# Kernel optimization log

Measured on AMD Instinct MI355X. Metric: run time of the kernel, lower is better.

## Reference

```python
import jax, jax.numpy as jnp
import numpy as np

N, D, K = 500000, 256, 64

def setup_inputs() -> dict:
    key = jax.random.key(0)
    kq, km = jax.random.split(key)
    query = jax.random.normal(kq, (D,), dtype=jnp.float32)
    mat = jax.random.normal(km, (N, D), dtype=jnp.float32)
    return {"query": query, "mat": mat, "k": K}

def reference(query, mat, k):
    # scores = mat @ query  : [N]
    scores = jnp.einsum("nd,d->n", mat, query)
    # top-k selection over all stored vectors
    _, idx = jax.lax.top_k(scores, k)
    # gather the selected rows : [k, D]
    out = jnp.take(mat, idx, axis=0)
    # idx stands in for the metadata gather (meta[i] for i in idx)
    return out, idx
```

## Files before the change

### kernel.cpp

```cpp
#include <hip/hip_runtime.h>
#include <stdint.h>

#define DIM 256
#define TOPK 64
#define HIST_BINS 65536
#define CAP 4096

__device__ __forceinline__ uint32_t fkey(float f) {
  uint32_t u = __float_as_uint(f);
  return (u & 0x80000000u) ? ~u : (u | 0x80000000u);
}

__global__ __launch_bounds__(256) void zero_kernel(uint32_t* __restrict__ hist,
                                                   int* __restrict__ cnt) {
  int tid = blockIdx.x * 256 + threadIdx.x;
  ((uint4*)hist)[tid] = make_uint4(0u, 0u, 0u, 0u);
  if (tid == 0) *cnt = 0;
}

__global__ __launch_bounds__(256) void score_kernel(
    const float* __restrict__ mat, const float* __restrict__ query,
    float* __restrict__ scores, uint32_t* __restrict__ hist, int n) {
  const int lane = threadIdx.x & 63;
  const int li = lane & 15;
  const int sub = lane >> 4;
  const int gw = blockIdx.x * 4 + (threadIdx.x >> 6);
  const int W = gridDim.x * 4;

  float4 q0 = ((const float4*)query)[li];
  float4 q1 = ((const float4*)query)[li + 16];
  float4 q2 = ((const float4*)query)[li + 32];
  float4 q3 = ((const float4*)query)[li + 48];

  int n4 = (n + 3) >> 2;
  for (int r4 = gw; r4 < n4; r4 += W) {
    int row = r4 * 4 + sub;
    float d = 0.f;
    if (row < n) {
      const float4* m4 = (const float4*)(mat + (size_t)row * DIM);
      float4 a = m4[li];
      float4 b = m4[li + 16];
      float4 c = m4[li + 32];
      float4 e = m4[li + 48];
      d = a.x * q0.x + a.y * q0.y + a.z * q0.z + a.w * q0.w;
      d += b.x * q1.x + b.y * q1.y + b.z * q1.z + b.w * q1.w;
      d += c.x * q2.x + c.y * q2.y + c.z * q2.z + c.w * q2.w;
      d += e.x * q3.x + e.y * q3.y + e.z * q3.z + e.w * q3.w;
    }
#pragma unroll
    for (int off = 8; off > 0; off >>= 1) d += __shfl_xor(d, off, 64);
    if (li == 0 && row < n) {
      scores[row] = d;
      atomicAdd(&hist[fkey(d) >> 16], 1u);
    }
  }
}

__global__ __launch_bounds__(256) void thresh_kernel(
    const uint32_t* __restrict__ hist, int* __restrict__ tbin) {
  __shared__ uint32_t s[256];
  __shared__ int fc;
  __shared__ uint32_t above;
  int t = threadIdx.x;

  uint32_t acc = 0;
  const uint4* h4 = (const uint4*)(hist + t * 256);
  for (int j = 0; j < 64; ++j) {
    uint4 v = h4[j];
    acc += v.x + v.y + v.z + v.w;
  }
  s[t] = acc;
  __syncthreads();
  for (int off = 1; off < 256; off <<= 1) {
    uint32_t v = (t + off < 256) ? s[t + off] : 0u;
    __syncthreads();
    s[t] += v;
    __syncthreads();
  }
  if (s[t] >= TOPK && (t == 255 || s[t + 1] < TOPK)) {
    fc = t;
    above = (t == 255) ? 0u : s[t + 1];
  }
  __syncthreads();
  int c = fc;
  uint32_t a = above;
  uint32_t h = hist[c * 256 + t];
  __syncthreads();
  s[t] = h;
  __syncthreads();
  for (int off = 1; off < 256; off <<= 1) {
    uint32_t v = (t + off < 256) ? s[t + off] : 0u;
    __syncthreads();
    s[t] += v;
    __syncthreads();
  }
  if (a + s[t] >= TOPK && (t == 255 || a + s[t + 1] < TOPK)) {
    *tbin = c * 256 + t;
  }
}

__global__ __launch_bounds__(256) void collect_kernel(
    const float* __restrict__ scores, const int* __restrict__ tbin,
    int* __restrict__ cnt, unsigned long long* __restrict__ cand, int n) {
  uint32_t T = (uint32_t)(*tbin);
  int i = blockIdx.x * 256 + threadIdx.x;
  int stride = gridDim.x * 256;
  for (; i < n; i += stride) {
    uint32_t key = fkey(scores[i]);
    if ((key >> 16) >= T) {
      int pos = atomicAdd(cnt, 1);
      if (pos < CAP) {
        cand[pos] = ((unsigned long long)key << 32) | (uint32_t)(~(uint32_t)i);
      }
    }
  }
}

__global__ __launch_bounds__(1024) void final_kernel(
    const unsigned long long* __restrict__ cand, const int* __restrict__ cnt,
    const float* __restrict__ mat, float* __restrict__ out) {
  __shared__ unsigned long long c[CAP];
  __shared__ int sel[TOPK];
  int t = threadIdx.x;
  int M = *cnt;
  if (M > CAP) M = CAP;

  for (int i = t; i < M; i += 1024) c[i] = cand[i];
  __syncthreads();

  for (int i = t; i < M; i += 1024) {
    unsigned long long mykey = c[i];
    int rank = 0;
    for (int j = 0; j < M; ++j) rank += (c[j] > mykey) ? 1 : 0;
    if (rank < TOPK) sel[rank] = (int)(~(uint32_t)(mykey & 0xFFFFFFFFull));
  }
  __syncthreads();

  if (t < TOPK) out[TOPK * DIM + t] = (float)sel[t];

  int wv = t >> 6, lane = t & 63;
  for (int r = wv; r < TOPK; r += 16) {
    size_t row = (size_t)sel[r];
    float4 v = ((const float4*)(mat + row * DIM))[lane];
    ((float4*)(out + r * DIM))[lane] = v;
  }
}

extern "C" void kernel_launch(void* const* d_in, const int* in_sizes, int n_in,
                              void* d_out, int out_size, void* d_ws, size_t ws_size,
                              hipStream_t stream) {
  const float* query = (const float*)d_in[0];
  const float* mat = (const float*)d_in[1];
  float* out = (float*)d_out;
  int n = in_sizes[1] / DIM;

  char* ws = (char*)d_ws;
  float* scores = (float*)ws;
  uint32_t* hist = (uint32_t*)(ws + (2u << 20));
  int* tbin = (int*)(ws + (2u << 20) + HIST_BINS * 4);
  int* cnt = tbin + 1;
  unsigned long long* cand =
      (unsigned long long*)(ws + (2u << 20) + HIST_BINS * 4 + 16);

  zero_kernel<<<64, 256, 0, stream>>>(hist, cnt);
  score_kernel<<<2048, 256, 0, stream>>>(mat, query, scores, hist, n);
  thresh_kernel<<<1, 256, 0, stream>>>(hist, tbin);
  collect_kernel<<<512, 256, 0, stream>>>(scores, tbin, cnt, cand, n);
  final_kernel<<<1, 1024, 0, stream>>>(cand, cnt, mat, out);
}
```

Before: 765.5 us.

## Process two rows per subgroup in scoring and fuse threshold into collect

The score kernel now has each 16-lane subgroup load and reduce two rows per iteration, putting more loads in flight. The grid size is computed from n rather than fixed. The single-block threshold kernel is removed and every collect block recomputes the threshold bin from the histogram, which saves one launch and its serialisation. The cost is that all 512 collect blocks each read the 256KB histogram redundantly.

```diff
diff --git a/kernel.cpp b/kernel.cpp
--- a/kernel.cpp
+++ b/kernel.cpp
@@ -9,6 +9,10 @@
 __device__ __forceinline__ uint32_t fkey(float f) {
   uint32_t u = __float_as_uint(f);
   return (u & 0x80000000u) ? ~u : (u | 0x80000000u);
+}
+
+__device__ __forceinline__ float dot4(float4 a, float4 q) {
+  return a.x * q.x + a.y * q.y + a.z * q.z + a.w * q.w;
 }
 
 __global__ __launch_bounds__(256) void zero_kernel(uint32_t* __restrict__ hist,
@@ -32,35 +36,48 @@
   float4 q2 = ((const float4*)query)[li + 32];
   float4 q3 = ((const float4*)query)[li + 48];
 
-  int n4 = (n + 3) >> 2;
-  for (int r4 = gw; r4 < n4; r4 += W) {
-    int row = r4 * 4 + sub;
-    float d = 0.f;
-    if (row < n) {
-      const float4* m4 = (const float4*)(mat + (size_t)row * DIM);
-      float4 a = m4[li];
-      float4 b = m4[li + 16];
-      float4 c = m4[li + 32];
-      float4 e = m4[li + 48];
-      d = a.x * q0.x + a.y * q0.y + a.z * q0.z + a.w * q0.w;
-      d += b.x * q1.x + b.y * q1.y + b.z * q1.z + b.w * q1.w;
-      d += c.x * q2.x + c.y * q2.y + c.z * q2.z + c.w * q2.w;
-      d += e.x * q3.x + e.y * q3.y + e.z * q3.z + e.w * q3.w;
+  int n8 = (n + 7) >> 3;
+  for (int r8 = gw; r8 < n8; r8 += W) {
+    int rowA = r8 * 8 + sub;
+    int rowB = rowA + 4;
+    float dA = 0.f, dB = 0.f;
+    if (rowB < n) {
+      const float4* mA = (const float4*)(mat + (size_t)rowA * DIM);
+      const float4* mB = (const float4*)(mat + (size_t)rowB * DIM);
+      float4 a0 = mA[li], a1 = mA[li + 16], a2 = mA[li + 32], a3 = mA[li + 48];
+      float4 b0 = mB[li], b1 = mB[li + 16], b2 = mB[li + 32], b3 = mB[li + 48];
+      dA = dot4(a0, q0) + dot4(a1, q1) + dot4(a2, q2) + dot4(a3, q3);
+      dB = dot4(b0, q0) + dot4(b1, q1) + dot4(b2, q2) + dot4(b3, q3);
+    } else if (rowA < n) {
+      const float4* mA = (const float4*)(mat + (size_t)rowA * DIM);
+      float4 a0 = mA[li], a1 = mA[li + 16], a2 = mA[li + 32], a3 = mA[li + 48];
+      dA = dot4(a0, q0) + dot4(a1, q1) + dot4(a2, q2) + dot4(a3, q3);
     }
 #pragma unroll
-    for (int off = 8; off > 0; off >>= 1) d += __shfl_xor(d, off, 64);
-    if (li == 0 && row < n) {
-      scores[row] = d;
-      atomicAdd(&hist[fkey(d) >> 16], 1u);
+    for (int off = 8; off > 0; off >>= 1) {
+      dA += __shfl_xor(dA, off, 64);
+      dB += __shfl_xor(dB, off, 64);
+    }
+    if (li == 0) {
+      if (rowA < n) {
+        scores[rowA] = dA;
+        atomicAdd(&hist[fkey(dA) >> 16], 1u);
+      }
+      if (rowB < n) {
+        scores[rowB] = dB;
+        atomicAdd(&hist[fkey(dB) >> 16], 1u);
+      }
     }
   }
 }
 
-__global__ __launch_bounds__(256) void thresh_kernel(
-    const uint32_t* __restrict__ hist, int* __restrict__ tbin) {
+__global__ __launch_bounds__(256) void collect_kernel(
+    const float* __restrict__ scores, const uint32_t* __restrict__ hist,
+    int* __restrict__ cnt, unsigned long long* __restrict__ cand, int n) {
   __shared__ uint32_t s[256];
   __shared__ int fc;
   __shared__ uint32_t above;
+  __shared__ int tb;
   int t = threadIdx.x;
 
   uint32_t acc = 0;
@@ -95,15 +112,12 @@
     __syncthreads();
   }
   if (a + s[t] >= TOPK && (t == 255 || a + s[t + 1] < TOPK)) {
-    *tbin = c * 256 + t;
+    tb = c * 256 + t;
   }
-}
+  __syncthreads();
+  uint32_t T = (uint32_t)tb;
 
-__global__ __launch_bounds__(256) void collect_kernel(
-    const float* __restrict__ scores, const int* __restrict__ tbin,
-    int* __restrict__ cnt, unsigned long long* __restrict__ cand, int n) {
-  uint32_t T = (uint32_t)(*tbin);
-  int i = blockIdx.x * 256 + threadIdx.x;
+  int i = blockIdx.x * 256 + t;
   int stride = gridDim.x * 256;
   for (; i < n; i += stride) {
     uint32_t key = fkey(scores[i]);
@@ -162,9 +176,12 @@
   unsigned long long* cand =
       (unsigned long long*)(ws + (2u << 20) + HIST_BINS * 4 + 16);
 
+  int n8 = (n + 7) >> 3;
+  int iters = (n8 + 8191) / 8192;
+  int sblocks = (n8 + 4 * iters - 1) / (4 * iters);
+
   zero_kernel<<<64, 256, 0, stream>>>(hist, cnt);
-  score_kernel<<<2048, 256, 0, stream>>>(mat, query, scores, hist, n);
-  thresh_kernel<<<1, 256, 0, stream>>>(hist, tbin);
-  collect_kernel<<<512, 256, 0, stream>>>(scores, tbin, cnt, cand, n);
+  score_kernel<<<sblocks, 256, 0, stream>>>(mat, query, scores, hist, n);
+  collect_kernel<<<512, 256, 0, stream>>>(scores, hist, cnt, cand, n);
   final_kernel<<<1, 1024, 0, stream>>>(cand, cnt, mat, out);
 }
```

New measurement: 771.2 us. About the same (+0.7%).

## Fuse threshold search into collect kernel and use nontemporal loads for scoring

Applied to the files above, without the earlier changes.

Removes the single-block threshold kernel launch by having every collect block redundantly scan the histogram to find the threshold bin in shared memory. The score kernel also switches matrix loads to nontemporal vector loads so the streamed matrix is meant to bypass cache retention. The trade-off is that 512 blocks each re-read the 256 KB histogram and run two scans, adding redundant work and traffic in exchange for one fewer launch and its serialization.

```diff
diff --git a/kernel.cpp b/kernel.cpp
--- a/kernel.cpp
+++ b/kernel.cpp
@@ -6,9 +6,15 @@
 #define HIST_BINS 65536
 #define CAP 4096
 
+typedef float f4 __attribute__((ext_vector_type(4)));
+
 __device__ __forceinline__ uint32_t fkey(float f) {
   uint32_t u = __float_as_uint(f);
   return (u & 0x80000000u) ? ~u : (u | 0x80000000u);
+}
+
+__device__ __forceinline__ float dot4v(f4 a, f4 q) {
+  return a[0] * q[0] + a[1] * q[1] + a[2] * q[2] + a[3] * q[3];
 }
 
 __global__ __launch_bounds__(256) void zero_kernel(uint32_t* __restrict__ hist,
@@ -27,25 +33,23 @@
   const int gw = blockIdx.x * 4 + (threadIdx.x >> 6);
   const int W = gridDim.x * 4;
 
-  float4 q0 = ((const float4*)query)[li];
-  float4 q1 = ((const float4*)query)[li + 16];
-  float4 q2 = ((const float4*)query)[li + 32];
-  float4 q3 = ((const float4*)query)[li + 48];
+  const f4* q4 = (const f4*)query;
+  f4 q0 = q4[li];
+  f4 q1 = q4[li + 16];
+  f4 q2 = q4[li + 32];
+  f4 q3 = q4[li + 48];
 
   int n4 = (n + 3) >> 2;
   for (int r4 = gw; r4 < n4; r4 += W) {
     int row = r4 * 4 + sub;
     float d = 0.f;
     if (row < n) {
-      const float4* m4 = (const float4*)(mat + (size_t)row * DIM);
-      float4 a = m4[li];
-      float4 b = m4[li + 16];
-      float4 c = m4[li + 32];
-      float4 e = m4[li + 48];
-      d = a.x * q0.x + a.y * q0.y + a.z * q0.z + a.w * q0.w;
-      d += b.x * q1.x + b.y * q1.y + b.z * q1.z + b.w * q1.w;
-      d += c.x * q2.x + c.y * q2.y + c.z * q2.z + c.w * q2.w;
-      d += e.x * q3.x + e.y * q3.y + e.z * q3.z + e.w * q3.w;
+      const f4* m4 = (const f4*)(mat + (size_t)row * DIM);
+      f4 a = __builtin_nontemporal_load(m4 + li);
+      f4 b = __builtin_nontemporal_load(m4 + li + 16);
+      f4 c = __builtin_nontemporal_load(m4 + li + 32);
+      f4 e = __builtin_nontemporal_load(m4 + li + 48);
+      d = dot4v(a, q0) + dot4v(b, q1) + dot4v(c, q2) + dot4v(e, q3);
     }
 #pragma unroll
     for (int off = 8; off > 0; off >>= 1) d += __shfl_xor(d, off, 64);
@@ -56,11 +60,13 @@
   }
 }
 
-__global__ __launch_bounds__(256) void thresh_kernel(
-    const uint32_t* __restrict__ hist, int* __restrict__ tbin) {
+__global__ __launch_bounds__(256) void collect_kernel(
+    const float* __restrict__ scores, const uint32_t* __restrict__ hist,
+    int* __restrict__ cnt, unsigned long long* __restrict__ cand, int n) {
   __shared__ uint32_t s[256];
   __shared__ int fc;
   __shared__ uint32_t above;
+  __shared__ int tb;
   int t = threadIdx.x;
 
   uint32_t acc = 0;
@@ -95,15 +101,12 @@
     __syncthreads();
   }
   if (a + s[t] >= TOPK && (t == 255 || a + s[t + 1] < TOPK)) {
-    *tbin = c * 256 + t;
+    tb = c * 256 + t;
   }
-}
+  __syncthreads();
+  uint32_t T = (uint32_t)tb;
 
-__global__ __launch_bounds__(256) void collect_kernel(
-    const float* __restrict__ scores, const int* __restrict__ tbin,
-    int* __restrict__ cnt, unsigned long long* __restrict__ cand, int n) {
-  uint32_t T = (uint32_t)(*tbin);
-  int i = blockIdx.x * 256 + threadIdx.x;
+  int i = blockIdx.x * 256 + t;
   int stride = gridDim.x * 256;
   for (; i < n; i += stride) {
     uint32_t key = fkey(scores[i]);
@@ -164,7 +167,6 @@
 
   zero_kernel<<<64, 256, 0, stream>>>(hist, cnt);
   score_kernel<<<2048, 256, 0, stream>>>(mat, query, scores, hist, n);
-  thresh_kernel<<<1, 256, 0, stream>>>(hist, tbin);
-  collect_kernel<<<512, 256, 0, stream>>>(scores, tbin, cnt, cand, n);
+  collect_kernel<<<512, 256, 0, stream>>>(scores, hist, cnt, cand, n);
   final_kernel<<<1, 1024, 0, stream>>>(cand, cnt, mat, out);
 }
```

Result: slower. 800.2 us (+4.5%).
